# Kernel tuning notes

Measured on AMD Instinct MI355X. Metric: run time of the kernel, lower is better.

The kernel has to match this reference:

```python
import jax, jax.numpy as jnp
import numpy as np

N_NODES = 100000
N_EDGES = 600000
EMB = 128
L = 5
NUM_ATOM = 119
NUM_CHIR = 3
NUM_BTYPE = 5
NUM_BDIR = 3
BN_EPS = 1e-5


def setup_inputs() -> dict:
    key = jax.random.key(0)
    ks = jax.random.split(key, 16)
    inp = {}
    inp['x'] = jax.random.randint(ks[0], (N_NODES, 2), 0, NUM_ATOM, dtype=jnp.int64 if jax.config.jax_enable_x64 else jnp.int32)
    inp['edge_index'] = jax.random.randint(ks[1], (2, N_EDGES), 0, N_NODES)
    inp['edge_attr'] = jax.random.randint(ks[2], (N_EDGES, 2), 0, NUM_BDIR)
    s = 0.05
    inp['x_emb1'] = jax.random.normal(ks[3], (NUM_ATOM, EMB), jnp.float32) * s
    inp['x_emb2'] = jax.random.normal(ks[4], (NUM_CHIR, EMB), jnp.float32) * s
    inp['edge_emb1'] = jax.random.normal(ks[5], (L, NUM_BTYPE, EMB), jnp.float32) * s
    inp['edge_emb2'] = jax.random.normal(ks[6], (L, NUM_BDIR, EMB), jnp.float32) * s
    inp['W1'] = jax.random.normal(ks[7], (L, EMB, 2 * EMB), jnp.float32) * (1.0 / np.sqrt(EMB))
    inp['b1'] = jnp.zeros((L, 2 * EMB), jnp.float32)
    inp['W2'] = jax.random.normal(ks[8], (L, 2 * EMB, EMB), jnp.float32) * (1.0 / np.sqrt(2 * EMB))
    inp['b2'] = jnp.zeros((L, EMB), jnp.float32)
    inp['eps'] = jnp.zeros((L,), jnp.float32)
    inp['gamma'] = jnp.ones((L, EMB), jnp.float32)
    inp['beta'] = jnp.zeros((L, EMB), jnp.float32)
    return inp


def reference(x, edge_index, edge_attr, x_emb1, x_emb2, edge_emb1, edge_emb2,
              W1, b1, W2, b2, eps, gamma, beta):
    N = x.shape[0]
    # node embedding: sum of two table lookups
    x0 = jnp.clip(x[:, 0], 0, x_emb1.shape[0] - 1)
    x1 = jnp.clip(x[:, 1], 0, x_emb2.shape[0] - 1)
    h = x_emb1[x0] + x_emb2[x1]  # [N, EMB]
    # add self loops (loop edge_attr = zeros -> bond type 0 / dir 0)
    loop = jnp.arange(N, dtype=edge_index.dtype)
    src = jnp.concatenate([edge_index[0], loop])  # [E+N]
    dst = jnp.concatenate([edge_index[1], loop])
    ea = jnp.concatenate([edge_attr, jnp.zeros((N, 2), dtype=edge_attr.dtype)], axis=0)
    e0 = jnp.clip(ea[:, 0], 0, edge_emb1.shape[1] - 1)
    e1 = jnp.clip(ea[:, 1], 0, edge_emb2.shape[1] - 1)
    n_layers = eps.shape[0]
    for i in range(n_layers):
        e = edge_emb1[i][e0] + edge_emb2[i][e1]              # [E+N, EMB]
        m = jax.nn.relu(h[src] + e)                           # gather + elementwise
        agg = jax.ops.segment_sum(m, dst, num_segments=N)     # scatter-add
        out = (1.0 + eps[i]) * h + agg
        # MLP: Linear -> ReLU -> Linear
        hmid = jax.nn.relu(out @ W1[i] + b1[i])
        h = hmid @ W2[i] + b2[i]
        # BatchNorm1d over nodes (batch statistics, biased variance)
        mean = jnp.mean(h, axis=0)
        var = jnp.mean((h - mean) ** 2, axis=0)
        h = (h - mean) * jax.lax.rsqrt(var + BN_EPS) * gamma[i] + beta[i]
        if i < n_layers - 1:
            h = jax.nn.relu(h)
    return h
```

## Files before the change

kernel.cpp:

```cpp
#include <hip/hip_runtime.h>

#define NN 100000
#define NPAD 100096
#define NE 600000
#define EMB 128

typedef unsigned short u16;
typedef unsigned int u32;
typedef unsigned long long u64;
typedef _Float16 half8 __attribute__((ext_vector_type(8)));
typedef float f32x4 __attribute__((ext_vector_type(4)));

__device__ __forceinline__ float4 ld4(const float* p) { return *(const float4*)p; }
__device__ __forceinline__ u32 packh2(float a, float b) {
  union { _Float16 h[2]; u32 d; } u;
  u.h[0] = (_Float16)a;
  u.h[1] = (_Float16)b;
  return u.d;
}

__global__ __launch_bounds__(256) void node_init_kernel(
    const int* __restrict__ x, const float* __restrict__ emb1,
    const float* __restrict__ emb2, _Float16* __restrict__ hb) {
  int tid = blockIdx.x * blockDim.x + threadIdx.x;
  int n = tid >> 4;
  if (n >= NN) return;
  int kc = tid & 15;
  int x0 = min(max(x[2 * n], 0), 118);
  int x1 = min(max(x[2 * n + 1], 0), 2);
  const float* p1 = emb1 + (size_t)x0 * EMB + kc * 8;
  const float* p2 = emb2 + (size_t)x1 * EMB + kc * 8;
  _Float16 o[8];
#pragma unroll
  for (int j = 0; j < 8; ++j) o[j] = (_Float16)(p1[j] + p2[j]);
  *(ulonglong2*)(hb + (size_t)n * EMB + kc * 8) = *(ulonglong2*)o;
}

__global__ __launch_bounds__(256) void hist_kernel(const int* __restrict__ ei,
                                                   int* __restrict__ deg) {
  int e = blockIdx.x * blockDim.x + threadIdx.x;
  if (e >= NE) return;
  atomicAdd(&deg[ei[NE + e]], 1);
}

__global__ __launch_bounds__(256) void scan1_kernel(const int* __restrict__ deg,
                                                    int* __restrict__ off,
                                                    int* __restrict__ bsum) {
  __shared__ int s[256];
  int t = threadIdx.x;
  int base = blockIdx.x * 1024 + t * 4;
  int v[4];
#pragma unroll
  for (int j = 0; j < 4; ++j) {
    int idx = base + j;
    v[j] = (idx < NN) ? deg[idx] : 0;
  }
  int tsum = v[0] + v[1] + v[2] + v[3];
  s[t] = tsum;
  __syncthreads();
  for (int d = 1; d < 256; d <<= 1) {
    int add = (t >= d) ? s[t - d] : 0;
    __syncthreads();
    s[t] += add;
    __syncthreads();
  }
  int run = s[t] - tsum;
#pragma unroll
  for (int j = 0; j < 4; ++j) {
    int idx = base + j;
    if (idx < NN) off[idx] = run;
    run += v[j];
  }
  if (t == 255) bsum[blockIdx.x] = s[255];
}

__global__ void scan2_kernel(int* __restrict__ bsum, int* __restrict__ off, int nb) {
  if (threadIdx.x == 0) {
    int run = 0;
    for (int b = 0; b < nb; ++b) {
      int v = bsum[b];
      bsum[b] = run;
      run += v;
    }
    off[NN] = run;
  }
}

__global__ __launch_bounds__(256) void scan3_kernel(int* __restrict__ off,
                                                    const int* __restrict__ bsum) {
  int idx = blockIdx.x * blockDim.x + threadIdx.x;
  if (idx < NN) off[idx] += bsum[idx >> 10];
}

__global__ __launch_bounds__(256) void scatter_kernel(
    const int* __restrict__ ei, const int* __restrict__ ea,
    const int* __restrict__ off, int* __restrict__ cnt, int* __restrict__ csr) {
  int e = blockIdx.x * blockDim.x + threadIdx.x;
  if (e >= NE) return;
  int d = ei[NE + e];
  int s = ei[e];
  int a0 = min(max(ea[2 * e], 0), 4);
  int a1 = min(max(ea[2 * e + 1], 0), 2);
  int code = a0 * 3 + a1;
  int r = atomicAdd(&cnt[d], 1);
  csr[off[d] + r] = s | (code << 20);
}

__global__ __launch_bounds__(256) void combo_kernel(const float* __restrict__ ee1,
                                                    const float* __restrict__ ee2,
                                                    float* __restrict__ combos) {
  int idx = blockIdx.x * blockDim.x + threadIdx.x;
  if (idx >= 5 * 15 * 128) return;
  int l = idx / (15 * 128);
  int rem = idx % (15 * 128);
  int code = rem / 128;
  int f = rem % 128;
  combos[idx] = ee1[(l * 5 + code / 3) * 128 + f] + ee2[(l * 3 + code % 3) * 128 + f];
}

__global__ __launch_bounds__(256) void prep_w_kernel(
    const float* __restrict__ W1g, const float* __restrict__ W2g,
    _Float16* __restrict__ W1f, _Float16* __restrict__ W2f) {
  int idx = blockIdx.x * blockDim.x + threadIdx.x;
  if (idx >= 40960) return;
  _Float16 o[8];
  if (idx < 20480) {
    int lane = idx & 63;
    int r = idx >> 6;
    int nt = r & 3, kt = (r >> 2) & 3, c = (r >> 4) & 3, l = r >> 6;
    int n = c * 64 + nt * 16 + (lane & 15);
    int kb = kt * 32 + (lane >> 4) * 8;
#pragma unroll
    for (int j = 0; j < 8; ++j) o[j] = (_Float16)W1g[((size_t)l * 128 + kb + j) * 256 + n];
    *(ulonglong2*)(W1f + (size_t)idx * 8) = *(ulonglong2*)o;
  } else {
    int i2 = idx - 20480;
    int lane = i2 & 63;
    int r = i2 >> 6;
    int nt = r & 7, ktl = (r >> 3) & 1, c = (r >> 4) & 3, l = r >> 6;
    int n = nt * 16 + (lane & 15);
    int kb = c * 64 + ktl * 32 + (lane >> 4) * 8;
#pragma unroll
    for (int j = 0; j < 8; ++j) o[j] = (_Float16)W2g[((size_t)l * 256 + kb + j) * 128 + n];
    *(ulonglong2*)(W2f + (size_t)i2 * 8) = *(ulonglong2*)o;
  }
}

template <bool NORM>
__global__ __launch_bounds__(256) void agg_kernel(
    const _Float16* __restrict__ hsrc, const float* __restrict__ scsh,
    const int* __restrict__ off, const int* __restrict__ csr,
    const float* __restrict__ cb, const float* __restrict__ epsp,
    _Float16* __restrict__ Af) {
  int tid = blockIdx.x * blockDim.x + threadIdx.x;
  int g = tid >> 4;
  int kc = tid & 15;
  float av[8] = {0.f, 0.f, 0.f, 0.f, 0.f, 0.f, 0.f, 0.f};
  float scv[8], shv[8];
  if (NORM) {
    float4 sa = ld4(scsh + kc * 8), sb = ld4(scsh + kc * 8 + 4);
    float4 ha = ld4(scsh + 128 + kc * 8), hbv = ld4(scsh + 128 + kc * 8 + 4);
    scv[0] = sa.x; scv[1] = sa.y; scv[2] = sa.z; scv[3] = sa.w;
    scv[4] = sb.x; scv[5] = sb.y; scv[6] = sb.z; scv[7] = sb.w;
    shv[0] = ha.x; shv[1] = ha.y; shv[2] = ha.z; shv[3] = ha.w;
    shv[4] = hbv.x; shv[5] = hbv.y; shv[6] = hbv.z; shv[7] = hbv.w;
  }
  if (g < NN) {
    const float eps1 = 1.0f + *epsp;
    ulonglong2 hraw = *(const ulonglong2*)(hsrc + (size_t)g * EMB + kc * 8);
    _Float16* hr = (_Float16*)&hraw;
    float4 ca = ld4(cb + kc * 8), cbv = ld4(cb + kc * 8 + 4);
    float cs[8] = {ca.x, ca.y, ca.z, ca.w, cbv.x, cbv.y, cbv.z, cbv.w};
#pragma unroll
    for (int j = 0; j < 8; ++j) {
      float hv = (float)hr[j];
      if (NORM) hv = fmaxf(hv * scv[j] + shv[j], 0.f);
      av[j] = eps1 * hv + fmaxf(hv + cs[j], 0.f);
    }
    int s0 = off[g], s1 = off[g + 1];
    int e = s0;
    for (; e + 3 < s1; e += 4) {
      int p0 = csr[e], p1 = csr[e + 1], p2 = csr[e + 2], p3 = csr[e + 3];
      ulonglong2 r0 = *(const ulonglong2*)(hsrc + (size_t)(p0 & 0xFFFFF) * EMB + kc * 8);
      ulonglong2 r1 = *(const ulonglong2*)(hsrc + (size_t)(p1 & 0xFFFFF) * EMB + kc * 8);
      ulonglong2 r2 = *(const ulonglong2*)(hsrc + (size_t)(p2 & 0xFFFFF) * EMB + kc * 8);
      ulonglong2 r3 = *(const ulonglong2*)(hsrc + (size_t)(p3 & 0xFFFFF) * EMB + kc * 8);
      ulonglong2 rr[4] = {r0, r1, r2, r3};
      int pp[4] = {p0, p1, p2, p3};
#pragma unroll
      for (int u = 0; u < 4; ++u) {
        const float* cp = cb + (size_t)(pp[u] >> 20) * EMB + kc * 8;
        float4 c0 = ld4(cp), c1 = ld4(cp + 4);
        float cc[8] = {c0.x, c0.y, c0.z, c0.w, c1.x, c1.y, c1.z, c1.w};
        _Float16* sp = (_Float16*)&rr[u];
#pragma unroll
        for (int j = 0; j < 8; ++j) {
          float v = (float)sp[j];
          if (NORM) v = fmaxf(v * scv[j] + shv[j], 0.f);
          av[j] += fmaxf(v + cc[j], 0.f);
        }
      }
    }
    for (; e < s1; ++e) {
      int p0 = csr[e];
      ulonglong2 r0 = *(const ulonglong2*)(hsrc + (size_t)(p0 & 0xFFFFF) * EMB + kc * 8);
      const float* cp = cb + (size_t)(p0 >> 20) * EMB + kc * 8;
      float4 c0 = ld4(cp), c1 = ld4(cp + 4);
      float cc[8] = {c0.x, c0.y, c0.z, c0.w, c1.x, c1.y, c1.z, c1.w};
      _Float16* sp = (_Float16*)&r0;
#pragma unroll
      for (int j = 0; j < 8; ++j) {
        float v = (float)sp[j];
        if (NORM) v = fmaxf(v * scv[j] + shv[j], 0.f);
        av[j] += fmaxf(v + cc[j], 0.f);
      }
    }
  }
  _Float16 o[8];
#pragma unroll
  for (int j = 0; j < 8; ++j) o[j] = (_Float16)av[j];
  *(ulonglong2*)(Af + (size_t)g * EMB + kc * 8) = *(ulonglong2*)o;
}

__global__ __launch_bounds__(256, 4) void mlp_kernel(
    const _Float16* __restrict__ Af, const _Float16* __restrict__ W1f,
    const _Float16* __restrict__ W2f,
    const float* __restrict__ b1g, const float* __restrict__ b2g,
    _Float16* __restrict__ hpre, float* __restrict__ slots) {
  __shared__ __align__(16) _Float16 Ws[16 * 64 * 8];

  const int t = threadIdx.x;
  const int w = t >> 6;
  const int lane = t & 63;
  const int q = lane >> 4, l15 = lane & 15;
  const int gw = blockIdx.x * 4 + w;
  const int n0 = gw * 16;
  float* sums = slots + (size_t)(gw & 31) * 256;

  half8 nh[4];
#pragma unroll
  for (int kt = 0; kt < 4; ++kt)
    nh[kt] = *(const half8*)(Af + (size_t)(n0 + l15) * EMB + kt * 32 + q * 8);

  f32x4 oacc[8];
#pragma unroll
  for (int a = 0; a < 8; ++a) oacc[a] = (f32x4){0.f, 0.f, 0.f, 0.f};

  const int srcA = ((q & 1) * 2) * 16 + l15;
  const int srcB = srcA + 16;
  const bool sel = (q >> 1) != 0;

  for (int c = 0; c < 4; ++c) {
    __syncthreads();
    {
      const _Float16* gb = W1f + ((size_t)(c * 16 + w * 4) * 64 + lane) * 8;
#pragma unroll
      for (int j = 0; j < 4; ++j)
        *(ulonglong2*)&Ws[(w * 4 + j) * 512 + lane * 8] =
            *(const ulonglong2*)(gb + (size_t)j * 512);
    }
    __syncthreads();

    f32x4 hacc[4];
#pragma unroll
    for (int a = 0; a < 4; ++a) hacc[a] = (f32x4){0.f, 0.f, 0.f, 0.f};
#pragma unroll
    for (int kt = 0; kt < 4; ++kt) {
#pragma unroll
      for (int colt = 0; colt < 4; ++colt) {
        half8 wh = *(const half8*)&Ws[(kt * 4 + colt) * 512 + lane * 8];
        hacc[colt] = __builtin_amdgcn_mfma_f32_16x16x32_f16(wh, nh[kt], hacc[colt], 0, 0, 0);
      }
    }
    __syncthreads();

    {
      const _Float16* gb = W2f + ((size_t)(c * 16 + w * 4) * 64 + lane) * 8;
#pragma unroll
      for (int j = 0; j < 4; ++j)
        *(ulonglong2*)&Ws[(w * 4 + j) * 512 + lane * 8] =
            *(const ulonglong2*)(gb + (size_t)j * 512);
    }

    u32 P01[4], P23[4];
#pragma unroll
    for (int colt = 0; colt < 4; ++colt) {
      float4 b1v = ld4(b1g + c * 64 + colt * 16 + q * 4);
      float v0 = fmaxf(hacc[colt][0] + b1v.x, 0.f);
      float v1 = fmaxf(hacc[colt][1] + b1v.y, 0.f);
      float v2 = fmaxf(hacc[colt][2] + b1v.z, 0.f);
      float v3 = fmaxf(hacc[colt][3] + b1v.w, 0.f);
      P01[colt] = packh2(v0, v1);
      P23[colt] = packh2(v2, v3);
    }
    __syncthreads();

#pragma unroll
    for (int ktl = 0; ktl < 2; ++ktl) {
      half8 bh;
      {
        union { u32 d[4]; half8 s; } uh;
        int c0 = 2 * ktl, c1 = 2 * ktl + 1;
        u32 a0, a1;
        a0 = (u32)__shfl((int)P01[c0], srcA); a1 = (u32)__shfl((int)P01[c1], srcA);
        uh.d[0] = sel ? a1 : a0;
        a0 = (u32)__shfl((int)P23[c0], srcA); a1 = (u32)__shfl((int)P23[c1], srcA);
        uh.d[1] = sel ? a1 : a0;
        a0 = (u32)__shfl((int)P01[c0], srcB); a1 = (u32)__shfl((int)P01[c1], srcB);
        uh.d[2] = sel ? a1 : a0;
        a0 = (u32)__shfl((int)P23[c0], srcB); a1 = (u32)__shfl((int)P23[c1], srcB);
        uh.d[3] = sel ? a1 : a0;
        bh = uh.s;
      }
#pragma unroll
      for (int nt = 0; nt < 8; ++nt) {
        half8 wh = *(const half8*)&Ws[(ktl * 8 + nt) * 512 + lane * 8];
        oacc[nt] = __builtin_amdgcn_mfma_f32_16x16x32_f16(wh, bh, oacc[nt], 0, 0, 0);
      }
    }
  }

  const int node = n0 + l15;
#pragma unroll
  for (int nt = 0; nt < 8; ++nt) {
    int ocb = nt * 16 + q * 4;
    float4 b2v = ld4(b2g + ocb);
    f32x4 s = (f32x4){0.f, 0.f, 0.f, 0.f};
    f32x4 s2 = (f32x4){0.f, 0.f, 0.f, 0.f};
    if (node < NN) {
      float v0 = oacc[nt][0] + b2v.x;
      float v1 = oacc[nt][1] + b2v.y;
      float v2 = oacc[nt][2] + b2v.z;
      float v3 = oacc[nt][3] + b2v.w;
      u64 pk = (u64)packh2(v0, v1) | ((u64)packh2(v2, v3) << 32);
      *(u64*)(hpre + (size_t)node * EMB + ocb) = pk;
      s[0] = v0; s[1] = v1; s[2] = v2; s[3] = v3;
      s2[0] = v0 * v0; s2[1] = v1 * v1; s2[2] = v2 * v2; s2[3] = v3 * v3;
    }
#pragma unroll
    for (int d = 1; d < 16; d <<= 1) {
#pragma unroll
      for (int r = 0; r < 4; ++r) {
        s[r] += __shfl_xor(s[r], d);
        s2[r] += __shfl_xor(s2[r], d);
      }
    }
    if (l15 == 0) {
#pragma unroll
      for (int r = 0; r < 4; ++r) {
        atomicAdd(&sums[ocb + r], s[r]);
        atomicAdd(&sums[128 + ocb + r], s2[r]);
      }
    }
  }
}

__global__ void stats_kernel(const float* __restrict__ slots,
                             const float* __restrict__ gamma,
                             const float* __restrict__ beta,
                             float* __restrict__ scsh) {
  int f = threadIdx.x;
  float s = 0.f, s2 = 0.f;
#pragma unroll 8
  for (int k = 0; k < 32; ++k) {
    s += slots[k * 256 + f];
    s2 += slots[k * 256 + 128 + f];
  }
  float mean = s * (1.0f / NN);
  float var = s2 * (1.0f / NN) - mean * mean;
  float sc = gamma[f] * rsqrtf(var + 1e-5f);
  scsh[f] = sc;
  scsh[128 + f] = beta[f] - mean * sc;
}

__global__ __launch_bounds__(256) void out_kernel(
    const _Float16* __restrict__ hpre, const float* __restrict__ scsh,
    float* __restrict__ out) {
  int tid = blockIdx.x * blockDim.x + threadIdx.x;
  int n = tid >> 4;
  if (n >= NN) return;
  int kc = tid & 15;
  ulonglong2 raw = *(const ulonglong2*)(hpre + (size_t)n * EMB + kc * 8);
  _Float16* hr = (_Float16*)&raw;
  float4 sa = ld4(scsh + kc * 8), sb = ld4(scsh + kc * 8 + 4);
  float4 ha = ld4(scsh + 128 + kc * 8), hbv = ld4(scsh + 128 + kc * 8 + 4);
  float scv[8] = {sa.x, sa.y, sa.z, sa.w, sb.x, sb.y, sb.z, sb.w};
  float shv[8] = {ha.x, ha.y, ha.z, ha.w, hbv.x, hbv.y, hbv.z, hbv.w};
  float v[8];
#pragma unroll
  for (int j = 0; j < 8; ++j) v[j] = (float)hr[j] * scv[j] + shv[j];
  float* d = out + (size_t)n * EMB + kc * 8;
  *(float4*)d = make_float4(v[0], v[1], v[2], v[3]);
  *(float4*)(d + 4) = make_float4(v[4], v[5], v[6], v[7]);
}

extern "C" void kernel_launch(void* const* d_in, const int* in_sizes, int n_in,
                              void* d_out, int out_size, void* d_ws, size_t ws_size,
                              hipStream_t stream) {
  const int* x = (const int*)d_in[0];
  const int* ei = (const int*)d_in[1];
  const int* ea = (const int*)d_in[2];
  const float* x_emb1 = (const float*)d_in[3];
  const float* x_emb2 = (const float*)d_in[4];
  const float* ee1 = (const float*)d_in[5];
  const float* ee2 = (const float*)d_in[6];
  const float* W1 = (const float*)d_in[7];
  const float* b1 = (const float*)d_in[8];
  const float* W2 = (const float*)d_in[9];
  const float* b2 = (const float*)d_in[10];
  const float* eps = (const float*)d_in[11];
  const float* gamma = (const float*)d_in[12];
  const float* beta = (const float*)d_in[13];
  float* out = (float*)d_out;

  float* slots = (float*)d_ws;
  float* scsh = slots + 5 * 32 * 256;
  float* combos = scsh + 5 * 256;
  _Float16* hpre = (_Float16*)(combos + 9600);
  _Float16* Af = hpre + (size_t)NN * EMB;
  _Float16* hb = Af + (size_t)NPAD * EMB;
  _Float16* W1f = hb + (size_t)NN * EMB;
  _Float16* W2f = W1f + 5 * 32768;
  int* deg = (int*)(W2f + 5 * 32768);
  int* off = deg + NN;
  int* csr = off + NN + 1;
  int* bsum = csr + NE;

  const int NB_SCAN = (NN + 1023) / 1024;

  hipMemsetAsync(deg, 0, NN * sizeof(int), stream);
  hipMemsetAsync(slots, 0, 5 * 32 * 256 * sizeof(float), stream);
  hist_kernel<<<(NE + 255) / 256, 256, 0, stream>>>(ei, deg);
  scan1_kernel<<<NB_SCAN, 256, 0, stream>>>(deg, off, bsum);
  scan2_kernel<<<1, 64, 0, stream>>>(bsum, off, NB_SCAN);
  scan3_kernel<<<(NN + 255) / 256, 256, 0, stream>>>(off, bsum);
  hipMemsetAsync(deg, 0, NN * sizeof(int), stream);
  scatter_kernel<<<(NE + 255) / 256, 256, 0, stream>>>(ei, ea, off, deg, csr);
  combo_kernel<<<(5 * 15 * 128 + 255) / 256, 256, 0, stream>>>(ee1, ee2, combos);
  prep_w_kernel<<<160, 256, 0, stream>>>(W1, W2, W1f, W2f);
  node_init_kernel<<<NN * 16 / 256 + 1, 256, 0, stream>>>(x, x_emb1, x_emb2, hb);

  const int NBLK = NPAD / 64;
  for (int i = 0; i < 5; ++i) {
    if (i == 0)
      agg_kernel<false><<<NPAD * 16 / 256, 256, 0, stream>>>(
          hb, nullptr, off, csr, combos + (size_t)i * 15 * EMB, eps + i, Af);
    else
      agg_kernel<true><<<NPAD * 16 / 256, 256, 0, stream>>>(
          hpre, scsh + (size_t)(i - 1) * 256, off, csr,
          combos + (size_t)i * 15 * EMB, eps + i, Af);
    mlp_kernel<<<NBLK, 256, 0, stream>>>(
        Af, W1f + (size_t)i * 32768, W2f + (size_t)i * 32768,
        b1 + (size_t)i * 256, b2 + (size_t)i * 128, hpre,
        slots + (size_t)i * 32 * 256);
    stats_kernel<<<1, 128, 0, stream>>>(slots + (size_t)i * 32 * 256,
                                        gamma + (size_t)i * EMB,
                                        beta + (size_t)i * EMB,
                                        scsh + (size_t)i * 256);
  }
  out_kernel<<<NN * 16 / 256 + 1, 256, 0, stream>>>(hpre, scsh + 4 * 256, out);
}
```

Measured before the change: 672.0 us.

## Stage full MLP weights in LDS once per block and process two node tiles per wave

```diff
diff --git a/kernel.cpp b/kernel.cpp
--- a/kernel.cpp
+++ b/kernel.cpp
@@ -222,120 +222,139 @@
   *(ulonglong2*)(Af + (size_t)g * EMB + kc * 8) = *(ulonglong2*)o;
 }
 
-__global__ __launch_bounds__(256, 4) void mlp_kernel(
+__global__ __launch_bounds__(512, 2) void mlp_kernel(
     const _Float16* __restrict__ Af, const _Float16* __restrict__ W1f,
     const _Float16* __restrict__ W2f,
     const float* __restrict__ b1g, const float* __restrict__ b2g,
     _Float16* __restrict__ hpre, float* __restrict__ slots) {
-  __shared__ __align__(16) _Float16 Ws[16 * 64 * 8];
+  extern __shared__ __align__(16) _Float16 Ws[];
+  _Float16* W1s = Ws;
+  _Float16* W2s = Ws + 32768;
 
   const int t = threadIdx.x;
   const int w = t >> 6;
   const int lane = t & 63;
   const int q = lane >> 4, l15 = lane & 15;
-  const int gw = blockIdx.x * 4 + w;
-  const int n0 = gw * 16;
+  const int gw = blockIdx.x * 8 + w;
+  const int n0 = blockIdx.x * 256 + w * 32;
   float* sums = slots + (size_t)(gw & 31) * 256;
 
-  half8 nh[4];
-#pragma unroll
-  for (int kt = 0; kt < 4; ++kt)
-    nh[kt] = *(const half8*)(Af + (size_t)(n0 + l15) * EMB + kt * 32 + q * 8);
-
-  f32x4 oacc[8];
-#pragma unroll
-  for (int a = 0; a < 8; ++a) oacc[a] = (f32x4){0.f, 0.f, 0.f, 0.f};
+  half8 nh[2][4];
+#pragma unroll
+  for (int ntile = 0; ntile < 2; ++ntile)
+#pragma unroll
+    for (int kt = 0; kt < 4; ++kt)
+      nh[ntile][kt] =
+          *(const half8*)(Af + (size_t)(n0 + ntile * 16 + l15) * EMB + kt * 32 + q * 8);
+
+  {
+    ulonglong2* d1 = (ulonglong2*)W1s;
+    ulonglong2* d2 = (ulonglong2*)W2s;
+    const ulonglong2* g1 = (const ulonglong2*)W1f;
+    const ulonglong2* g2 = (const ulonglong2*)W2f;
+#pragma unroll
+    for (int j = 0; j < 8; ++j) d1[t + j * 512] = g1[t + j * 512];
+#pragma unroll
+    for (int j = 0; j < 8; ++j) d2[t + j * 512] = g2[t + j * 512];
+  }
+  __syncthreads();
+
+  f32x4 oacc[2][8];
+#pragma unroll
+  for (int ntile = 0; ntile < 2; ++ntile)
+#pragma unroll
+    for (int a = 0; a < 8; ++a) oacc[ntile][a] = (f32x4){0.f, 0.f, 0.f, 0.f};
 
   const int srcA = ((q & 1) * 2) * 16 + l15;
   const int srcB = srcA + 16;
   const bool sel = (q >> 1) != 0;
 
   for (int c = 0; c < 4; ++c) {
-    __syncthreads();
-    {
-      const _Float16* gb = W1f + ((size_t)(c * 16 + w * 4) * 64 + lane) * 8;
-#pragma unroll
-      for (int j = 0; j < 4; ++j)
-        *(ulonglong2*)&Ws[(w * 4 + j) * 512 + lane * 8] =
-            *(const ulonglong2*)(gb + (size_t)j * 512);
-    }
-    __syncthreads();
-
-    f32x4 hacc[4];
-#pragma unroll
-    for (int a = 0; a < 4; ++a) hacc[a] = (f32x4){0.f, 0.f, 0.f, 0.f};
+    f32x4 hacc[2][4];
+#pragma unroll
+    for (int ntile = 0; ntile < 2; ++ntile)
+#pragma unroll
+      for (int a = 0; a < 4; ++a) hacc[ntile][a] = (f32x4){0.f, 0.f, 0.f, 0.f};
 #pragma unroll
     for (int kt = 0; kt < 4; ++kt) {
+      half8 wh[4];
+#pragma unroll
+      for (int colt = 0; colt < 4; ++colt)
+        wh[colt] = *(const half8*)&W1s[(c * 16 + kt * 4 + colt) * 512 + lane * 8];
 #pragma unroll
       for (int colt = 0; colt < 4; ++colt) {
-        half8 wh = *(const half8*)&Ws[(kt * 4 + colt) * 512 + lane * 8];
-        hacc[colt] = __builtin_amdgcn_mfma_f32_16x16x32_f16(wh, nh[kt], hacc[colt], 0, 0, 0);
-      }
-    }
-    __syncthreads();
-
-    {
-      const _Float16* gb = W2f + ((size_t)(c * 16 + w * 4) * 64 + lane) * 8;
-#pragma unroll
-      for (int j = 0; j < 4; ++j)
-        *(ulonglong2*)&Ws[(w * 4 + j) * 512 + lane * 8] =
-            *(const ulonglong2*)(gb + (size_t)j * 512);
-    }
-
-    u32 P01[4], P23[4];
+        hacc[0][colt] =
+            __builtin_amdgcn_mfma_f32_16x16x32_f16(wh[colt], nh[0][kt], hacc[0][colt], 0, 0, 0);
+        hacc[1][colt] =
+            __builtin_amdgcn_mfma_f32_16x16x32_f16(wh[colt], nh[1][kt], hacc[1][colt], 0, 0, 0);
+      }
+    }
+
+    u32 P01[2][4], P23[2][4];
 #pragma unroll
     for (int colt = 0; colt < 4; ++colt) {
       float4 b1v = ld4(b1g + c * 64 + colt * 16 + q * 4);
-      float v0 = fmaxf(hacc[colt][0] + b1v.x, 0.f);
-      float v1 = fmaxf(hacc[colt][1] + b1v.y, 0.f);
-      float v2 = fmaxf(hacc[colt][2] + b1v.z, 0.f);
-      float v3 = fmaxf(hacc[colt][3] + b1v.w, 0.f);
-      P01[colt] = packh2(v0, v1);
-      P23[colt] = packh2(v2, v3);
-    }
-    __syncthreads();
+#pragma unroll
+      for (int ntile = 0; ntile < 2; ++ntile) {
+        float v0 = fmaxf(hacc[ntile][colt][0] + b1v.x, 0.f);
+        float v1 = fmaxf(hacc[ntile][colt][1] + b1v.y, 0.f);
+        float v2 = fmaxf(hacc[ntile][colt][2] + b1v.z, 0.f);
+        float v3 = fmaxf(hacc[ntile][colt][3] + b1v.w, 0.f);
+        P01[ntile][colt] = packh2(v0, v1);
+        P23[ntile][colt] = packh2(v2, v3);
+      }
+    }
 
 #pragma unroll
     for (int ktl = 0; ktl < 2; ++ktl) {
-      half8 bh;
-      {
+      half8 bh[2];
+#pragma unroll
+      for (int ntile = 0; ntile < 2; ++ntile) {
         union { u32 d[4]; half8 s; } uh;
         int c0 = 2 * ktl, c1 = 2 * ktl + 1;
         u32 a0, a1;
-        a0 = (u32)__shfl((int)P01[c0], srcA); a1 = (u32)__shfl((int)P01[c1], srcA);
+        a0 = (u32)__shfl((int)P01[ntile][c0], srcA);
+        a1 = (u32)__shfl((int)P01[ntile][c1], srcA);
         uh.d[0] = sel ? a1 : a0;
-        a0 = (u32)__shfl((int)P23[c0], srcA); a1 = (u32)__shfl((int)P23[c1], srcA);
+        a0 = (u32)__shfl((int)P23[ntile][c0], srcA);
+        a1 = (u32)__shfl((int)P23[ntile][c1], srcA);
         uh.d[1] = sel ? a1 : a0;
-        a0 = (u32)__shfl((int)P01[c0], srcB); a1 = (u32)__shfl((int)P01[c1], srcB);
+        a0 = (u32)__shfl((int)P01[ntile][c0], srcB);
+        a1 = (u32)__shfl((int)P01[ntile][c1], srcB);
         uh.d[2] = sel ? a1 : a0;
-        a0 = (u32)__shfl((int)P23[c0], srcB); a1 = (u32)__shfl((int)P23[c1], srcB);
+        a0 = (u32)__shfl((int)P23[ntile][c0], srcB);
+        a1 = (u32)__shfl((int)P23[ntile][c1], srcB);
         uh.d[3] = sel ? a1 : a0;
-        bh = uh.s;
+        bh[ntile] = uh.s;
       }
 #pragma unroll
       for (int nt = 0; nt < 8; ++nt) {
-        half8 wh = *(const half8*)&Ws[(ktl * 8 + nt) * 512 + lane * 8];
-        oacc[nt] = __builtin_amdgcn_mfma_f32_16x16x32_f16(wh, bh, oacc[nt], 0, 0, 0);
-      }
-    }
-  }
-
-  const int node = n0 + l15;
+        half8 wh = *(const half8*)&W2s[(c * 16 + ktl * 8 + nt) * 512 + lane * 8];
+        oacc[0][nt] = __builtin_amdgcn_mfma_f32_16x16x32_f16(wh, bh[0], oacc[0][nt], 0, 0, 0);
+        oacc[1][nt] = __builtin_amdgcn_mfma_f32_16x16x32_f16(wh, bh[1], oacc[1][nt], 0, 0, 0);
+      }
+    }
+  }
+
 #pragma unroll
   for (int nt = 0; nt < 8; ++nt) {
     int ocb = nt * 16 + q * 4;
     float4 b2v = ld4(b2g + ocb);
     f32x4 s = (f32x4){0.f, 0.f, 0.f, 0.f};
     f32x4 s2 = (f32x4){0.f, 0.f, 0.f, 0.f};
-    if (node < NN) {
-      float v0 = oacc[nt][0] + b2v.x;
-      float v1 = oacc[nt][1] + b2v.y;
-      float v2 = oacc[nt][2] + b2v.z;
-      float v3 = oacc[nt][3] + b2v.w;
-      u64 pk = (u64)packh2(v0, v1) | ((u64)packh2(v2, v3) << 32);
-      *(u64*)(hpre + (size_t)node * EMB + ocb) = pk;
-      s[0] = v0; s[1] = v1; s[2] = v2; s[3] = v3;
-      s2[0] = v0 * v0; s2[1] = v1 * v1; s2[2] = v2 * v2; s2[3] = v3 * v3;
+#pragma unroll
+    for (int ntile = 0; ntile < 2; ++ntile) {
+      int node = n0 + ntile * 16 + l15;
+      if (node < NN) {
+        float v0 = oacc[ntile][nt][0] + b2v.x;
+        float v1 = oacc[ntile][nt][1] + b2v.y;
+        float v2 = oacc[ntile][nt][2] + b2v.z;
+        float v3 = oacc[ntile][nt][3] + b2v.w;
+        u64 pk = (u64)packh2(v0, v1) | ((u64)packh2(v2, v3) << 32);
+        *(u64*)(hpre + (size_t)node * EMB + ocb) = pk;
+        s[0] += v0; s[1] += v1; s[2] += v2; s[3] += v3;
+        s2[0] += v0 * v0; s2[1] += v1 * v1; s2[2] += v2 * v2; s2[3] += v3 * v3;
+      }
     }
 #pragma unroll
     for (int d = 1; d < 16; d <<= 1) {
@@ -413,6 +432,13 @@
   const float* beta = (const float*)d_in[13];
   float* out = (float*)d_out;
 
+  static int _attr_once = []() {
+    hipFuncSetAttribute((const void*)mlp_kernel,
+                        hipFuncAttributeMaxDynamicSharedMemorySize, 131072);
+    return 0;
+  }();
+  (void)_attr_once;
+
   float* slots = (float*)d_ws;
   float* scsh = slots + 5 * 32 * 256;
   float* combos = scsh + 5 * 256;
@@ -440,7 +466,7 @@
   prep_w_kernel<<<160, 256, 0, stream>>>(W1, W2, W1f, W2f);
   node_init_kernel<<<NN * 16 / 256 + 1, 256, 0, stream>>>(x, x_emb1, x_emb2, hb);
 
-  const int NBLK = NPAD / 64;
+  const int MLP_GRID = NPAD / 256;
   for (int i = 0; i < 5; ++i) {
     if (i == 0)
       agg_kernel<false><<<NPAD * 16 / 256, 256, 0, stream>>>(
@@ -449,7 +475,7 @@
       agg_kernel<true><<<NPAD * 16 / 256, 256, 0, stream>>>(
           hpre, scsh + (size_t)(i - 1) * 256, off, csr,
           combos + (size_t)i * 15 * EMB, eps + i, Af);
-    mlp_kernel<<<NBLK, 256, 0, stream>>>(
+    mlp_kernel<<<MLP_GRID, 512, 131072, stream>>>(
         Af, W1f + (size_t)i * 32768, W2f + (size_t)i * 32768,
         b1 + (size_t)i * 256, b2 + (size_t)i * 128, hpre,
         slots + (size_t)i * 32 * 256);
```

Measured after the change: 673.0 us. Within noise of the previous version (+0.1%).
